# Kernel optimization log

Measured on AMD Instinct MI355X. Metric: run time of the kernel, lower is better.

## Reference

```python
import jax, jax.numpy as jnp
import numpy as np

B, C, HK, WK = 1, 128, 32, 32
S = 4                       # upsample factor hq/hk = dilation
HQ, WQ = HK * S, WK * S
NH = 4                      # heads
HD = C // NH                # head dim
KH = KW = 7                 # odd(max(3, round(2*0.1*32)))
DH = DW = S
EPS = float(jnp.finfo(jnp.float32).eps)  # torch RMSNorm default eps for fp32


def natten_indices(L, K, D):
    """NATTEN clamped-window key indices per query position. Returns [L, K] int array."""
    NS = K // 2
    i = np.arange(L)
    if D <= 1:
        start = np.maximum(i - NS, 0) + (i + NS >= L) * (L - i - NS - 1)
    else:
        ni = i - NS * D
        imodd = i % D
        a = (L // D) * D
        b = L - a
        far = np.where(imodd < b, L - b + imodd - 2 * NS * D, a + imodd - K * D)
        start = np.where(ni < 0, imodd, np.where(i + NS * D >= L, far, ni))
    return jnp.asarray(start[:, None] + np.arange(K)[None, :] * D)


def setup_inputs() -> dict:
    key = jax.random.key(0)
    ks = jax.random.split(key, 8)
    sc = 1.0 / np.sqrt(C)
    return {
        "q": jax.random.normal(ks[0], (B, C, HQ, WQ), jnp.float32),
        "k": jax.random.normal(ks[1], (B, C, HK, WK), jnp.float32),
        "v": jax.random.normal(ks[2], (B, C, HK, WK), jnp.float32),
        "conv_w": jax.random.normal(ks[3], (C, C, 3, 3), jnp.float32) * (sc / 3.0),
        "normq_w": 1.0 + 0.02 * jax.random.normal(ks[4], (C,), jnp.float32),
        "normk_w": 1.0 + 0.02 * jax.random.normal(ks[5], (C,), jnp.float32),
        "qproj_w": jax.random.normal(ks[6], (C, C), jnp.float32) * sc,
        "qproj_b": jnp.zeros((C,), jnp.float32),
        "kproj_w": jax.random.normal(ks[7], (C, C), jnp.float32) * sc,
        "kproj_b": jnp.zeros((C,), jnp.float32),
    }


def _rmsnorm(x, w):  # x: [B,C,H,W]; RMS over channel dim
    ms = jnp.mean(x * x, axis=1, keepdims=True)
    return x * jax.lax.rsqrt(ms + EPS) * w[None, :, None, None]


def reference(q, k, v, conv_w, normq_w, normk_w, qproj_w, qproj_b, kproj_w, kproj_b):
    # 3x3 conv on q (no bias, padding=1)
    q = jax.lax.conv_general_dilated(q, conv_w, (1, 1), "SAME",
                                     dimension_numbers=("NCHW", "OIHW", "NCHW"))
    q = _rmsnorm(q, normq_w)
    k = _rmsnorm(k, normk_w)
    # 1x1 projections (Conv2d k=1 with bias)
    q = jnp.einsum("oc,bchw->bohw", qproj_w, q) + qproj_b[None, :, None, None]
    k = jnp.einsum("oc,bchw->bohw", kproj_w, k) + kproj_b[None, :, None, None]
    # nearest-exact upsample of k, v to (HQ, WQ); integer factor -> exact pixel repeat
    k = jnp.repeat(jnp.repeat(k, S, axis=2), S, axis=3)
    v = jnp.repeat(jnp.repeat(v, S, axis=2), S, axis=3)
    # NATTEN layout [B, H, W, heads, hd]
    qn = q.reshape(B, NH, HD, HQ, WQ).transpose(0, 3, 4, 1, 2)
    kn = k.reshape(B, NH, HD, HQ, WQ).transpose(0, 3, 4, 1, 2)
    vh = v.transpose(0, 2, 3, 1)  # [B,HQ,WQ,C]; V is shared (expanded) across heads.
    # channel-pad-to-8 in the original is a no-op here since C % 8 == 0.
    ih = natten_indices(HQ, KH, DH)  # [HQ, KH]
    iw = natten_indices(WQ, KW, DW)  # [WQ, KW]
    k_nb = jnp.take(jnp.take(kn, ih, axis=1), iw, axis=3)  # [B,HQ,KH,WQ,KW,NH,HD]
    v_nb = jnp.take(jnp.take(vh, ih, axis=1), iw, axis=3)  # [B,HQ,KH,WQ,KW,C]
    scale = HD ** -0.5
    logits = jnp.einsum("bijhd,bimjnhd->bijhmn", qn, k_nb) * scale
    attn = jax.nn.softmax(logits.reshape(B, HQ, WQ, NH, KH * KW), axis=-1)
    attn = attn.reshape(B, HQ, WQ, NH, KH, KW)
    # heads share V, and the block takes mean over heads at the end; the mean
    # commutes with the (linear) V-contraction, so average attention first.
    attn_mean = attn.mean(axis=3)  # [B,HQ,WQ,KH,KW]
    out = jnp.einsum("bijmn,bimjnc->bcij", attn_mean, v_nb)  # [B,C,HQ,WQ]
    return out
```

## Files before the change

### kernel.cpp

```cpp
#include <hip/hip_runtime.h>

#define EPS_ 1.1920928955078125e-07f
#define SCALE_ 0.17677669529663687f

typedef __attribute__((ext_vector_type(8))) short s8b;
typedef __attribute__((ext_vector_type(4))) float f32x4;

static __device__ __forceinline__ unsigned short f2bf(float f) {
  unsigned int u = __float_as_uint(f);
  unsigned int r = (u + 0x7fffu + ((u >> 16) & 1u)) >> 16;
  return (unsigned short)r;
}
static __device__ __forceinline__ float b2fs(short h) {
  return __uint_as_float(((unsigned int)(unsigned short)h) << 16);
}
static __device__ __forceinline__ int S_(int c) {
  return (c < 3) ? 0 : ((c > 28) ? 25 : (c - 3));
}

__global__ __launch_bounds__(256) void prep_k(
    const float* __restrict__ q_in, const float* __restrict__ k_in,
    const float* __restrict__ v_in, const float* __restrict__ conv_w,
    const float* __restrict__ normq_w, const float* __restrict__ normk_w,
    const float* __restrict__ qproj_w, const float* __restrict__ kproj_w,
    const float* __restrict__ kbias,
    unsigned short* __restrict__ qb, unsigned short* __restrict__ vb,
    unsigned short* __restrict__ kpb, unsigned short* __restrict__ wb,
    unsigned short* __restrict__ wnq) {
  __shared__ __align__(16) char smem[53504];
  unsigned short* t_l = (unsigned short*)smem;
  unsigned short* x_l = (unsigned short*)smem;
  unsigned short* wnk_l = (unsigned short*)(smem + 17408);
  float* red_l = (float*)(smem + 52224);
  float* rs_l  = (float*)(smem + 53248);
  const int b = blockIdx.x, tid = threadIdx.x;
  const int w = tid >> 6, lane = tid & 63;
  const int lm = lane & 15, kg = lane >> 4;

  if (b < 256) {
    const int px0 = b * 64;
    for (int i = tid; i < 2048; i += 256) {
      int c = i >> 4, f = i & 15;
      float4 v = *(const float4*)&q_in[c * 16384 + px0 + f * 4];
      t_l[(f * 4 + 0) * 136 + c] = f2bf(v.x);
      t_l[(f * 4 + 1) * 136 + c] = f2bf(v.y);
      t_l[(f * 4 + 2) * 136 + c] = f2bf(v.z);
      t_l[(f * 4 + 3) * 136 + c] = f2bf(v.w);
    }
    __syncthreads();
    for (int i = tid; i < 1024; i += 256) {
      int p = i >> 4, s = i & 15;
      int px = px0 + p;
      int opx = px + 2 * (px >> 7) + 131;
      *(s8b*)&qb[opx * 128 + s * 8] = *(const s8b*)&t_l[p * 136 + s * 8];
    }
  } else if (b < 265) {
    int gid = (b - 256) * 256 + tid;
    s8b z = {0, 0, 0, 0, 0, 0, 0, 0};
    for (int j = gid; j < 2080; j += 2304) {
      *(s8b*)&qb[j * 8] = z;
      *(s8b*)&qb[129 * 130 * 128 + j * 8] = z;
    }
    for (int j = gid; j < 2048; j += 2304) {
      int r = (j >> 4) + 1, s = j & 15;
      *(s8b*)&qb[(r * 130) * 128 + s * 8] = z;
      *(s8b*)&qb[(r * 130 + 129) * 128 + s * 8] = z;
    }
  } else if (b < 269) {
#pragma unroll
    for (int it = 0; it < 16; it++) {
      int ch8 = (b - 265) * 4096 + it * 256 + tid;
      const float4 v0 = *(const float4*)&v_in[ch8 * 8];
      const float4 v1 = *(const float4*)&v_in[ch8 * 8 + 4];
      s8b o;
      o[0] = (short)f2bf(v0.x); o[1] = (short)f2bf(v0.y);
      o[2] = (short)f2bf(v0.z); o[3] = (short)f2bf(v0.w);
      o[4] = (short)f2bf(v1.x); o[5] = (short)f2bf(v1.y);
      o[6] = (short)f2bf(v1.z); o[7] = (short)f2bf(v1.w);
      *(s8b*)&vb[ch8 * 8] = o;
    }
  } else if (b < 285) {
    const int px0 = (b - 269) * 64;
    for (int i = tid; i < 2048; i += 256) {
      int c = i >> 4, f = i & 15;
      float4 v = *(const float4*)&k_in[c * 1024 + px0 + f * 4];
      x_l[(f * 4 + 0) * 136 + c] = f2bf(v.x);
      x_l[(f * 4 + 1) * 136 + c] = f2bf(v.y);
      x_l[(f * 4 + 2) * 136 + c] = f2bf(v.z);
      x_l[(f * 4 + 3) * 136 + c] = f2bf(v.w);
    }
    for (int i = tid; i < 16384; i += 256) {
      int o = i >> 7, c = i & 127;
      wnk_l[o * 136 + c] = f2bf(kproj_w[i] * normk_w[c]);
    }
    __syncthreads();
    {
      int px = tid >> 2, t4 = tid & 3;
      float ssum = 0.f;
#pragma unroll
      for (int j = 0; j < 4; j++) {
        s8b v = *(const s8b*)&x_l[px * 136 + t4 * 32 + j * 8];
#pragma unroll
        for (int e = 0; e < 8; e++) { float f = b2fs(v[e]); ssum += f * f; }
      }
      red_l[px * 4 + t4] = ssum;
    }
    __syncthreads();
    if (tid < 64)
      rs_l[tid] = rsqrtf((red_l[4 * tid] + red_l[4 * tid + 1] + red_l[4 * tid + 2] +
                          red_l[4 * tid + 3]) * (1.f / 128.f) + EPS_);
    __syncthreads();
    f32x4 acc[2][4];
#pragma unroll
    for (int a = 0; a < 2; a++)
#pragma unroll
      for (int n = 0; n < 4; n++) acc[a][n] = (f32x4){0.f, 0.f, 0.f, 0.f};
#pragma unroll
    for (int kc = 0; kc < 4; kc++) {
      s8b a0 = *(const s8b*)&wnk_l[(2 * w * 16 + lm) * 136 + kc * 32 + kg * 8];
      s8b a1 = *(const s8b*)&wnk_l[((2 * w + 1) * 16 + lm) * 136 + kc * 32 + kg * 8];
#pragma unroll
      for (int nt = 0; nt < 4; nt++) {
        s8b bf = *(const s8b*)&x_l[(nt * 16 + lm) * 136 + kc * 32 + kg * 8];
        acc[0][nt] = __builtin_amdgcn_mfma_f32_16x16x32_bf16(a0, bf, acc[0][nt], 0, 0, 0);
        acc[1][nt] = __builtin_amdgcn_mfma_f32_16x16x32_bf16(a1, bf, acc[1][nt], 0, 0, 0);
      }
    }
    __syncthreads();
#pragma unroll
    for (int mi = 0; mi < 2; mi++)
#pragma unroll
      for (int nt = 0; nt < 4; nt++)
#pragma unroll
        for (int r = 0; r < 4; r++) {
          int px = nt * 16 + lm, c = (2 * w + mi) * 16 + kg * 4 + r;
          x_l[px * 136 + c] = f2bf(kbias[c] + rs_l[px] * acc[mi][nt][r]);
        }
    __syncthreads();
    for (int i = tid; i < 1024; i += 256) {
      int px = i >> 4, s = i & 15;
      *(s8b*)&kpb[(px0 + px) * 128 + s * 8] = *(const s8b*)&x_l[px * 136 + s * 8];
    }
  } else if (b < 349) {
    int g = (b - 285) * 256 + tid;
    int i32 = g & 31, oc = (g >> 5) & 127, kc = g >> 12;
    const float* src = conv_w + oc * 1152 + (kc * 32 + i32) * 9;
#pragma unroll
    for (int t = 0; t < 9; t++)
      wb[t * 16384 + g] = f2bf(src[t]);
  } else {
    int base = ((b - 349) * 256 + tid) * 8;
    const float4 v0 = *(const float4*)&qproj_w[base];
    const float4 v1 = *(const float4*)&qproj_w[base + 4];
    int c = base & 127;
    s8b o;
    o[0] = (short)f2bf(v0.x * normq_w[c + 0]); o[1] = (short)f2bf(v0.y * normq_w[c + 1]);
    o[2] = (short)f2bf(v0.z * normq_w[c + 2]); o[3] = (short)f2bf(v0.w * normq_w[c + 3]);
    o[4] = (short)f2bf(v1.x * normq_w[c + 4]); o[5] = (short)f2bf(v1.y * normq_w[c + 5]);
    o[6] = (short)f2bf(v1.z * normq_w[c + 6]); o[7] = (short)f2bf(v1.w * normq_w[c + 7]);
    *(s8b*)&wnq[base] = o;
  }
}

__global__ __launch_bounds__(512) void fused_k(
    const unsigned short* __restrict__ qb, const unsigned short* __restrict__ wb,
    const unsigned short* __restrict__ wnq, const float* __restrict__ qbias,
    const unsigned short* __restrict__ kpb, const unsigned short* __restrict__ vb,
    float* __restrict__ out) {
  __shared__ __align__(16) char smem[55552];
  unsigned short* in_l = (unsigned short*)smem;
  unsigned short* qc_l = (unsigned short*)smem;
  unsigned short* a_l  = (unsigned short*)smem;
  float* o_l = (float*)smem;
  unsigned short* v_l = (unsigned short*)(smem + 34816);
  float* red_l = (float*)(smem + 53248);
  float* rs_l  = (float*)(smem + 55296);

  const int tid = threadIdx.x;
  const int CY = blockIdx.x >> 4, CX = blockIdx.x & 15;
  const int Y0 = CY * 8, X0 = CX * 8;
  const int w = tid >> 6, lane = tid & 63;
  const int lm = lane & 15, kg = lane >> 4;
  const int wm = w >> 1, wn = w & 1;

  const int sy0 = S_(2 * CY), sy1 = S_(2 * CY + 1);
  const int sx0 = S_(2 * CX), sx1 = S_(2 * CX + 1);
  const int kyb = min(sy0, 24), kxb = min(sx0, 24);
  const int oy0 = sy0 - kyb, oy1 = sy1 - kyb;
  const int ox0 = sx0 - kxb, ox1 = sx1 - kxb;

  for (int i = tid; i < 1600; i += 512) {
    int s = i & 15, r = i >> 4;
    int ry = r / 10, rx = r - ry * 10;
    *(s8b*)&in_l[(ry * 12 + rx) * 136 + s * 8] =
        *(const s8b*)&qb[((Y0 + ry) * 130 + X0 + rx) * 128 + s * 8];
  }
  {
    const int kxe = kxb & ~1;
    for (int i = tid; i < 1024; i += 512) {
      int ch = i & 127, ky = i >> 7;
      const unsigned short* src = &vb[ch * 1024 + (kyb + ky) * 32 + kxe];
      s8b a = *(const s8b*)src;
      if (kxb & 1) {
        s8b bsec = *(const s8b*)(src + 8);
        s8b o;
#pragma unroll
        for (int e = 0; e < 7; e++) o[e] = a[e + 1];
        o[7] = bsec[0];
        *(s8b*)&v_l[ch * 72 + ky * 8] = o;
      } else {
        *(s8b*)&v_l[ch * 72 + ky * 8] = a;
      }
    }
  }
  __syncthreads();

  f32x4 acc[2][2];
#pragma unroll
  for (int a = 0; a < 2; a++)
#pragma unroll
    for (int n = 0; n < 2; n++) acc[a][n] = (f32x4){0.f, 0.f, 0.f, 0.f};
#pragma unroll
  for (int t = 0; t < 9; t++) {
    const int dy = t / 3, dx = t - (t / 3) * 3;
#pragma unroll
    for (int kc = 0; kc < 4; kc++) {
      const unsigned short* wp = wb + (t * 4 + kc) * 4096;
      s8b a0 = *(const s8b*)&wp[(wm * 32 + lm) * 32 + kg * 8];
      s8b a1 = *(const s8b*)&wp[(wm * 32 + 16 + lm) * 32 + kg * 8];
#pragma unroll
      for (int ni = 0; ni < 2; ni++) {
        int nt = wn * 2 + ni;
        int qy = 2 * nt + (lm >> 3), qx = lm & 7;
        s8b bf = *(const s8b*)&in_l[((qy + dy) * 12 + qx + dx) * 136 + kc * 32 + kg * 8];
        acc[0][ni] = __builtin_amdgcn_mfma_f32_16x16x32_bf16(a0, bf, acc[0][ni], 0, 0, 0);
        acc[1][ni] = __builtin_amdgcn_mfma_f32_16x16x32_bf16(a1, bf, acc[1][ni], 0, 0, 0);
      }
    }
  }
  __syncthreads();
#pragma unroll
  for (int mi = 0; mi < 2; mi++)
#pragma unroll
    for (int ni = 0; ni < 2; ni++)
#pragma unroll
      for (int r = 0; r < 4; r++) {
        int px = (wn * 2 + ni) * 16 + lm, c = wm * 32 + mi * 16 + kg * 4 + r;
        qc_l[px * 136 + c] = f2bf(acc[mi][ni][r]);
      }
  __syncthreads();

  {
    int px = tid >> 3, t8 = tid & 7;
    float ssum = 0.f;
#pragma unroll
    for (int j = 0; j < 2; j++) {
      s8b v = *(const s8b*)&qc_l[px * 136 + t8 * 16 + j * 8];
#pragma unroll
      for (int e = 0; e < 8; e++) { float f = b2fs(v[e]); ssum += f * f; }
    }
    red_l[px * 8 + t8] = ssum;
  }
  __syncthreads();
  if (tid < 64) {
    float4 r0 = *(const float4*)&red_l[tid * 8];
    float4 r1 = *(const float4*)&red_l[tid * 8 + 4];
    rs_l[tid] = rsqrtf((r0.x + r0.y + r0.z + r0.w + r1.x + r1.y + r1.z + r1.w) *
                           (1.f / 128.f) + EPS_);
  }
  __syncthreads();

  f32x4 acc2[2][2];
#pragma unroll
  for (int a = 0; a < 2; a++)
#pragma unroll
    for (int n = 0; n < 2; n++) acc2[a][n] = (f32x4){0.f, 0.f, 0.f, 0.f};
#pragma unroll
  for (int kc = 0; kc < 4; kc++) {
    s8b a0 = *(const s8b*)&wnq[(wm * 32 + lm) * 128 + kc * 32 + kg * 8];
    s8b a1 = *(const s8b*)&wnq[(wm * 32 + 16 + lm) * 128 + kc * 32 + kg * 8];
#pragma unroll
    for (int ni = 0; ni < 2; ni++) {
      s8b bf = *(const s8b*)&qc_l[((wn * 2 + ni) * 16 + lm) * 136 + kc * 32 + kg * 8];
      acc2[0][ni] = __builtin_amdgcn_mfma_f32_16x16x32_bf16(a0, bf, acc2[0][ni], 0, 0, 0);
      acc2[1][ni] = __builtin_amdgcn_mfma_f32_16x16x32_bf16(a1, bf, acc2[1][ni], 0, 0, 0);
    }
  }
  __syncthreads();
#pragma unroll
  for (int mi = 0; mi < 2; mi++)
#pragma unroll
    for (int ni = 0; ni < 2; ni++)
#pragma unroll
      for (int r = 0; r < 4; r++) {
        int px = (wn * 2 + ni) * 16 + lm, c = wm * 32 + mi * 16 + kg * 4 + r;
        qc_l[px * 136 + c] = f2bf(qbias[c] + rs_l[px] * acc2[mi][ni][r]);
      }
  __syncthreads();

  const int h = w >> 1, qh = w & 1;
  f32x4 lg[2][4];
  {
    s8b af[2], bfv[4];
#pragma unroll
    for (int i = 0; i < 2; i++)
      af[i] = *(const s8b*)&qc_l[((qh * 2 + i) * 16 + lm) * 136 + h * 32 + kg * 8];
#pragma unroll
    for (int nt = 0; nt < 4; nt++) {
      int n = nt * 16 + lm;
      int ky = n >> 3, kx = n & 7;
      bfv[nt] = *(const s8b*)&kpb[((kyb + ky) * 32 + kxb + kx) * 128 + h * 32 + kg * 8];
    }
#pragma unroll
    for (int i = 0; i < 2; i++)
#pragma unroll
      for (int nt = 0; nt < 4; nt++)
        lg[i][nt] = __builtin_amdgcn_mfma_f32_16x16x32_bf16(
            af[i], bfv[nt], (f32x4){0.f, 0.f, 0.f, 0.f}, 0, 0, 0);
  }
  __syncthreads();

  const int kyA = lm >> 3, kxq = lm & 7;
  const bool kxv0 = (unsigned)(kxq - ox0) < 7u;
  const bool kxv1 = (unsigned)(kxq - ox1) < 7u;
#pragma unroll
  for (int i = 0; i < 2; i++) {
    const int mt = qh * 2 + i;
#pragma unroll
    for (int r = 0; r < 4; r++) {
      int j = mt * 16 + kg * 4 + r;
      int oy = ((j >> 5) & 1) ? oy1 : oy0;
      bool kxv = ((j >> 2) & 1) ? kxv1 : kxv0;
      float l[4];
#pragma unroll
      for (int nt = 0; nt < 4; nt++) {
        int ky = 2 * nt + kyA;
        bool valid = kxv && ((unsigned)(ky - oy) < 7u);
        l[nt] = valid ? lg[i][nt][r] * SCALE_ : -1e30f;
      }
      float mx = fmaxf(fmaxf(l[0], l[1]), fmaxf(l[2], l[3]));
#pragma unroll
      for (int off = 1; off < 16; off <<= 1) mx = fmaxf(mx, __shfl_xor(mx, off, 64));
      float e0 = __expf(l[0] - mx), e1 = __expf(l[1] - mx);
      float e2 = __expf(l[2] - mx), e3 = __expf(l[3] - mx);
      float ss = e0 + e1 + e2 + e3;
#pragma unroll
      for (int off = 1; off < 16; off <<= 1) ss += __shfl_xor(ss, off, 64);
      float inv = 1.f / ss;
      unsigned short* ap = &a_l[(h * 64 + j) * 68];
      ap[lm] = f2bf(e0 * inv);
      ap[16 + lm] = f2bf(e1 * inv);
      ap[32 + lm] = f2bf(e2 * inv);
      ap[48 + lm] = f2bf(e3 * inv);
    }
  }
  __syncthreads();

  const int ph = w & 1, cb = w >> 1;
  f32x4 oacc[2][2];
#pragma unroll
  for (int a = 0; a < 2; a++)
#pragma unroll
    for (int n = 0; n < 2; n++) oacc[a][n] = (f32x4){0.f, 0.f, 0.f, 0.f};
#pragma unroll
  for (int kc = 0; kc < 2; kc++) {
    s8b bfr[2];
#pragma unroll
    for (int nt2 = 0; nt2 < 2; nt2++)
      bfr[nt2] = *(const s8b*)&v_l[(cb * 32 + nt2 * 16 + lm) * 72 + kc * 32 + kg * 8];
#pragma unroll
    for (int hh = 0; hh < 4; hh++) {
#pragma unroll
      for (int mi = 0; mi < 2; mi++) {
        s8b afr = *(const s8b*)&a_l[(hh * 64 + (ph * 2 + mi) * 16 + lm) * 68 + kc * 32 + kg * 8];
#pragma unroll
        for (int nt2 = 0; nt2 < 2; nt2++)
          oacc[mi][nt2] = __builtin_amdgcn_mfma_f32_16x16x32_bf16(afr, bfr[nt2], oacc[mi][nt2], 0, 0, 0);
      }
    }
  }
  __syncthreads();
#pragma unroll
  for (int mi = 0; mi < 2; mi++)
#pragma unroll
    for (int nt2 = 0; nt2 < 2; nt2++)
#pragma unroll
      for (int r = 0; r < 4; r++)
        o_l[(cb * 32 + nt2 * 16 + lm) * 68 + (ph * 2 + mi) * 16 + kg * 4 + r] =
            0.25f * oacc[mi][nt2][r];
  __syncthreads();
  for (int i = tid; i < 2048; i += 512) {
    int c = i >> 4, rr = i & 15;
    int qy = rr >> 1, hx = rr & 1;
    float4 v = *(const float4*)&o_l[c * 68 + qy * 8 + hx * 4];
    *(float4*)&out[c * 16384 + (Y0 + qy) * 128 + X0 + hx * 4] = v;
  }
}

extern "C" void kernel_launch(void* const* d_in, const int* in_sizes, int n_in,
                              void* d_out, int out_size, void* d_ws, size_t ws_size,
                              hipStream_t stream) {
  const float* q_in    = (const float*)d_in[0];
  const float* k_in    = (const float*)d_in[1];
  const float* v_in    = (const float*)d_in[2];
  const float* conv_w  = (const float*)d_in[3];
  const float* normq_w = (const float*)d_in[4];
  const float* normk_w = (const float*)d_in[5];
  const float* qproj_w = (const float*)d_in[6];
  const float* qproj_b = (const float*)d_in[7];
  const float* kproj_w = (const float*)d_in[8];
  const float* kproj_b = (const float*)d_in[9];
  float* out = (float*)d_out;

  char* ws = (char*)d_ws;
  unsigned short* qb  = (unsigned short*)(ws);
  unsigned short* vb  = (unsigned short*)(ws + 4326400);
  unsigned short* kpb = (unsigned short*)(ws + 4588544);
  unsigned short* wb  = (unsigned short*)(ws + 4850688);
  unsigned short* wnq = (unsigned short*)(ws + 5145600);

  prep_k<<<dim3(357), 256, 0, stream>>>(q_in, k_in, v_in, conv_w, normq_w, normk_w,
                                        qproj_w, kproj_w, kproj_b,
                                        qb, vb, kpb, wb, wnq);
  fused_k<<<dim3(256), 512, 0, stream>>>(qb, wb, wnq, qproj_b, kpb, vb, out);
}
```

Measured before the change: 109.4 us.

## Merge prep and fused kernels into one cooperative launch with grid sync

Fuses the bf16 prep kernel and the main attention kernel into a single cooperative kernel of 256 blocks × 512 threads. Every block first transposes its q slice, and the first 93 blocks also handle k projection, conv-weight, v, q-proj weight and padding work. A grid-wide barrier then separates this from the attention phase. This removes one kernel launch and the inter-kernel gap, at the cost of a grid sync and uneven prep work across blocks.

After: 162.5 us. 1.49x slower.

```diff
diff --git a/kernel.cpp b/kernel.cpp
--- a/kernel.cpp
+++ b/kernel.cpp
@@ -1,4 +1,7 @@
 #include <hip/hip_runtime.h>
+#include <hip/hip_cooperative_groups.h>
+
+namespace cg = cooperative_groups;
 
 #define EPS_ 1.1920928955078125e-07f
 #define SCALE_ 0.17677669529663687f
@@ -18,28 +21,25 @@
   return (c < 3) ? 0 : ((c > 28) ? 25 : (c - 3));
 }
 
-__global__ __launch_bounds__(256) void prep_k(
+__global__ __launch_bounds__(512) void natten_k(
     const float* __restrict__ q_in, const float* __restrict__ k_in,
     const float* __restrict__ v_in, const float* __restrict__ conv_w,
     const float* __restrict__ normq_w, const float* __restrict__ normk_w,
-    const float* __restrict__ qproj_w, const float* __restrict__ kproj_w,
-    const float* __restrict__ kbias,
+    const float* __restrict__ qproj_w, const float* __restrict__ qbias,
+    const float* __restrict__ kproj_w, const float* __restrict__ kbias,
     unsigned short* __restrict__ qb, unsigned short* __restrict__ vb,
     unsigned short* __restrict__ kpb, unsigned short* __restrict__ wb,
-    unsigned short* __restrict__ wnq) {
-  __shared__ __align__(16) char smem[53504];
-  unsigned short* t_l = (unsigned short*)smem;
-  unsigned short* x_l = (unsigned short*)smem;
-  unsigned short* wnk_l = (unsigned short*)(smem + 17408);
-  float* red_l = (float*)(smem + 52224);
-  float* rs_l  = (float*)(smem + 53248);
+    unsigned short* __restrict__ wnq, float* __restrict__ out) {
+  __shared__ __align__(16) char smem[55552];
   const int b = blockIdx.x, tid = threadIdx.x;
   const int w = tid >> 6, lane = tid & 63;
   const int lm = lane & 15, kg = lane >> 4;
-
-  if (b < 256) {
+  const int wm = w >> 1, wn = w & 1;
+
+  {
+    unsigned short* t_l = (unsigned short*)smem;
     const int px0 = b * 64;
-    for (int i = tid; i < 2048; i += 256) {
+    for (int i = tid; i < 2048; i += 512) {
       int c = i >> 4, f = i & 15;
       float4 v = *(const float4*)&q_in[c * 16384 + px0 + f * 4];
       t_l[(f * 4 + 0) * 136 + c] = f2bf(v.x);
@@ -48,40 +48,22 @@
       t_l[(f * 4 + 3) * 136 + c] = f2bf(v.w);
     }
     __syncthreads();
-    for (int i = tid; i < 1024; i += 256) {
+    for (int i = tid; i < 1024; i += 512) {
       int p = i >> 4, s = i & 15;
       int px = px0 + p;
       int opx = px + 2 * (px >> 7) + 131;
       *(s8b*)&qb[opx * 128 + s * 8] = *(const s8b*)&t_l[p * 136 + s * 8];
     }
-  } else if (b < 265) {
-    int gid = (b - 256) * 256 + tid;
-    s8b z = {0, 0, 0, 0, 0, 0, 0, 0};
-    for (int j = gid; j < 2080; j += 2304) {
-      *(s8b*)&qb[j * 8] = z;
-      *(s8b*)&qb[129 * 130 * 128 + j * 8] = z;
-    }
-    for (int j = gid; j < 2048; j += 2304) {
-      int r = (j >> 4) + 1, s = j & 15;
-      *(s8b*)&qb[(r * 130) * 128 + s * 8] = z;
-      *(s8b*)&qb[(r * 130 + 129) * 128 + s * 8] = z;
-    }
-  } else if (b < 269) {
-#pragma unroll
-    for (int it = 0; it < 16; it++) {
-      int ch8 = (b - 265) * 4096 + it * 256 + tid;
-      const float4 v0 = *(const float4*)&v_in[ch8 * 8];
-      const float4 v1 = *(const float4*)&v_in[ch8 * 8 + 4];
-      s8b o;
-      o[0] = (short)f2bf(v0.x); o[1] = (short)f2bf(v0.y);
-      o[2] = (short)f2bf(v0.z); o[3] = (short)f2bf(v0.w);
-      o[4] = (short)f2bf(v1.x); o[5] = (short)f2bf(v1.y);
-      o[6] = (short)f2bf(v1.z); o[7] = (short)f2bf(v1.w);
-      *(s8b*)&vb[ch8 * 8] = o;
-    }
-  } else if (b < 285) {
-    const int px0 = (b - 269) * 64;
-    for (int i = tid; i < 2048; i += 256) {
+    __syncthreads();
+  }
+
+  if (b < 16) {
+    unsigned short* x_l = (unsigned short*)smem;
+    unsigned short* wnk_l = (unsigned short*)(smem + 17408);
+    float* red_l = (float*)(smem + 52224);
+    float* rs_l  = (float*)(smem + 54272);
+    const int px0 = b * 64;
+    for (int i = tid; i < 2048; i += 512) {
       int c = i >> 4, f = i & 15;
       float4 v = *(const float4*)&k_in[c * 1024 + px0 + f * 4];
       x_l[(f * 4 + 0) * 136 + c] = f2bf(v.x);
@@ -89,67 +71,80 @@
       x_l[(f * 4 + 2) * 136 + c] = f2bf(v.z);
       x_l[(f * 4 + 3) * 136 + c] = f2bf(v.w);
     }
-    for (int i = tid; i < 16384; i += 256) {
+    for (int i = tid; i < 16384; i += 512) {
       int o = i >> 7, c = i & 127;
       wnk_l[o * 136 + c] = f2bf(kproj_w[i] * normk_w[c]);
     }
     __syncthreads();
     {
-      int px = tid >> 2, t4 = tid & 3;
+      int px = tid >> 3, t8 = tid & 7;
       float ssum = 0.f;
 #pragma unroll
-      for (int j = 0; j < 4; j++) {
-        s8b v = *(const s8b*)&x_l[px * 136 + t4 * 32 + j * 8];
+      for (int j = 0; j < 2; j++) {
+        s8b v = *(const s8b*)&x_l[px * 136 + t8 * 16 + j * 8];
 #pragma unroll
         for (int e = 0; e < 8; e++) { float f = b2fs(v[e]); ssum += f * f; }
       }
-      red_l[px * 4 + t4] = ssum;
-    }
-    __syncthreads();
-    if (tid < 64)
-      rs_l[tid] = rsqrtf((red_l[4 * tid] + red_l[4 * tid + 1] + red_l[4 * tid + 2] +
-                          red_l[4 * tid + 3]) * (1.f / 128.f) + EPS_);
-    __syncthreads();
-    f32x4 acc[2][4];
+      red_l[px * 8 + t8] = ssum;
+    }
+    __syncthreads();
+    if (tid < 64) {
+      float4 r0 = *(const float4*)&red_l[tid * 8];
+      float4 r1 = *(const float4*)&red_l[tid * 8 + 4];
+      rs_l[tid] = rsqrtf((r0.x + r0.y + r0.z + r0.w + r1.x + r1.y + r1.z + r1.w) *
+                             (1.f / 128.f) + EPS_);
+    }
+    __syncthreads();
+    f32x4 acc[2][2];
 #pragma unroll
     for (int a = 0; a < 2; a++)
 #pragma unroll
-      for (int n = 0; n < 4; n++) acc[a][n] = (f32x4){0.f, 0.f, 0.f, 0.f};
+      for (int n = 0; n < 2; n++) acc[a][n] = (f32x4){0.f, 0.f, 0.f, 0.f};
 #pragma unroll
     for (int kc = 0; kc < 4; kc++) {
-      s8b a0 = *(const s8b*)&wnk_l[(2 * w * 16 + lm) * 136 + kc * 32 + kg * 8];
-      s8b a1 = *(const s8b*)&wnk_l[((2 * w + 1) * 16 + lm) * 136 + kc * 32 + kg * 8];
-#pragma unroll
-      for (int nt = 0; nt < 4; nt++) {
-        s8b bf = *(const s8b*)&x_l[(nt * 16 + lm) * 136 + kc * 32 + kg * 8];
-        acc[0][nt] = __builtin_amdgcn_mfma_f32_16x16x32_bf16(a0, bf, acc[0][nt], 0, 0, 0);
-        acc[1][nt] = __builtin_amdgcn_mfma_f32_16x16x32_bf16(a1, bf, acc[1][nt], 0, 0, 0);
+      s8b a0 = *(const s8b*)&wnk_l[(wm * 32 + lm) * 136 + kc * 32 + kg * 8];
+      s8b a1 = *(const s8b*)&wnk_l[(wm * 32 + 16 + lm) * 136 + kc * 32 + kg * 8];
+#pragma unroll
+      for (int ni = 0; ni < 2; ni++) {
+        s8b bf = *(const s8b*)&x_l[((wn * 2 + ni) * 16 + lm) * 136 + kc * 32 + kg * 8];
+        acc[0][ni] = __builtin_amdgcn_mfma_f32_16x16x32_bf16(a0, bf, acc[0][ni], 0, 0, 0);
+        acc[1][ni] = __builtin_amdgcn_mfma_f32_16x16x32_bf16(a1, bf, acc[1][ni], 0, 0, 0);
       }
     }
     __syncthreads();
 #pragma unroll
     for (int mi = 0; mi < 2; mi++)
 #pragma unroll
-      for (int nt = 0; nt < 4; nt++)
+      for (int ni = 0; ni < 2; ni++)
 #pragma unroll
         for (int r = 0; r < 4; r++) {
-          int px = nt * 16 + lm, c = (2 * w + mi) * 16 + kg * 4 + r;
-          x_l[px * 136 + c] = f2bf(kbias[c] + rs_l[px] * acc[mi][nt][r]);
+          int px = (wn * 2 + ni) * 16 + lm, c = wm * 32 + mi * 16 + kg * 4 + r;
+          x_l[px * 136 + c] = f2bf(kbias[c] + rs_l[px] * acc[mi][ni][r]);
         }
     __syncthreads();
-    for (int i = tid; i < 1024; i += 256) {
+    for (int i = tid; i < 1024; i += 512) {
       int px = i >> 4, s = i & 15;
       *(s8b*)&kpb[(px0 + px) * 128 + s * 8] = *(const s8b*)&x_l[px * 136 + s * 8];
     }
-  } else if (b < 349) {
-    int g = (b - 285) * 256 + tid;
+  } else if (b < 48) {
+    int g = (b - 16) * 512 + tid;
     int i32 = g & 31, oc = (g >> 5) & 127, kc = g >> 12;
     const float* src = conv_w + oc * 1152 + (kc * 32 + i32) * 9;
 #pragma unroll
     for (int t = 0; t < 9; t++)
       wb[t * 16384 + g] = f2bf(src[t]);
-  } else {
-    int base = ((b - 349) * 256 + tid) * 8;
+  } else if (b < 80) {
+    int ch8 = (b - 48) * 512 + tid;
+    const float4 v0 = *(const float4*)&v_in[ch8 * 8];
+    const float4 v1 = *(const float4*)&v_in[ch8 * 8 + 4];
+    s8b o;
+    o[0] = (short)f2bf(v0.x); o[1] = (short)f2bf(v0.y);
+    o[2] = (short)f2bf(v0.z); o[3] = (short)f2bf(v0.w);
+    o[4] = (short)f2bf(v1.x); o[5] = (short)f2bf(v1.y);
+    o[6] = (short)f2bf(v1.z); o[7] = (short)f2bf(v1.w);
+    *(s8b*)&vb[ch8 * 8] = o;
+  } else if (b < 84) {
+    int base = ((b - 80) * 512 + tid) * 8;
     const float4 v0 = *(const float4*)&qproj_w[base];
     const float4 v1 = *(const float4*)&qproj_w[base + 4];
     int c = base & 127;
@@ -159,15 +154,23 @@
     o[4] = (short)f2bf(v1.x * normq_w[c + 4]); o[5] = (short)f2bf(v1.y * normq_w[c + 5]);
     o[6] = (short)f2bf(v1.z * normq_w[c + 6]); o[7] = (short)f2bf(v1.w * normq_w[c + 7]);
     *(s8b*)&wnq[base] = o;
-  }
-}
-
-__global__ __launch_bounds__(512) void fused_k(
-    const unsigned short* __restrict__ qb, const unsigned short* __restrict__ wb,
-    const unsigned short* __restrict__ wnq, const float* __restrict__ qbias,
-    const unsigned short* __restrict__ kpb, const unsigned short* __restrict__ vb,
-    float* __restrict__ out) {
-  __shared__ __align__(16) char smem[55552];
+  } else if (b < 93) {
+    int gid = (b - 84) * 512 + tid;
+    s8b z = {0, 0, 0, 0, 0, 0, 0, 0};
+    if (gid < 2080) {
+      *(s8b*)&qb[gid * 8] = z;
+      *(s8b*)&qb[129 * 130 * 128 + gid * 8] = z;
+    }
+    if (gid < 2048) {
+      int r = (gid >> 4) + 1, s = gid & 15;
+      *(s8b*)&qb[(r * 130) * 128 + s * 8] = z;
+      *(s8b*)&qb[(r * 130 + 129) * 128 + s * 8] = z;
+    }
+  }
+
+  __syncthreads();
+  cg::this_grid().sync();
+
   unsigned short* in_l = (unsigned short*)smem;
   unsigned short* qc_l = (unsigned short*)smem;
   unsigned short* a_l  = (unsigned short*)smem;
@@ -176,12 +179,8 @@
   float* red_l = (float*)(smem + 53248);
   float* rs_l  = (float*)(smem + 55296);
 
-  const int tid = threadIdx.x;
-  const int CY = blockIdx.x >> 4, CX = blockIdx.x & 15;
+  const int CY = b >> 4, CX = b & 15;
   const int Y0 = CY * 8, X0 = CX * 8;
-  const int w = tid >> 6, lane = tid & 63;
-  const int lm = lane & 15, kg = lane >> 4;
-  const int wm = w >> 1, wn = w & 1;
 
   const int sy0 = S_(2 * CY), sy1 = S_(2 * CY + 1);
   const int sx0 = S_(2 * CX), sx1 = S_(2 * CX + 1);
@@ -419,8 +418,11 @@
   unsigned short* wb  = (unsigned short*)(ws + 4850688);
   unsigned short* wnq = (unsigned short*)(ws + 5145600);
 
-  prep_k<<<dim3(357), 256, 0, stream>>>(q_in, k_in, v_in, conv_w, normq_w, normk_w,
-                                        qproj_w, kproj_w, kproj_b,
-                                        qb, vb, kpb, wb, wnq);
-  fused_k<<<dim3(256), 512, 0, stream>>>(qb, wb, wnq, qproj_b, kpb, vb, out);
+  void* args[] = {
+      (void*)&q_in, (void*)&k_in, (void*)&v_in, (void*)&conv_w,
+      (void*)&normq_w, (void*)&normk_w, (void*)&qproj_w, (void*)&qproj_b,
+      (void*)&kproj_w, (void*)&kproj_b,
+      (void*)&qb, (void*)&vb, (void*)&kpb, (void*)&wb, (void*)&wnq,
+      (void*)&out};
+  hipLaunchCooperativeKernel((void*)natten_k, dim3(256), dim3(512), args, 0, stream);
 }
```
